# Performance work log

Measured on AMD Instinct MI355X. Metric: run time of the kernel, lower is better.

Reference implementation:

```python
import jax, jax.numpy as jnp
from jax import lax
import numpy as np

S, B, H, E, A = 1024, 32, 512, 512, 256  # seq_len, batch, hid_dim, emb_dim, att_dim


def setup_inputs() -> dict:
    key = jax.random.key(0)
    ks = jax.random.split(key, 12)
    sc = 0.02
    return {
        "outs": jax.random.normal(ks[0], (S, B, H), dtype=jnp.float32),
        "emb": jax.random.normal(ks[1], (S, B, E), dtype=jnp.float32),
        # Bahdanau scorer params: enc projection (project_enc_outs), dec projection, score vector v
        "W_enc": jax.random.normal(ks[2], (A, E), dtype=jnp.float32) * sc,
        "b_enc": jnp.zeros((A,), dtype=jnp.float32),
        "W_dec": jax.random.normal(ks[3], (A, H), dtype=jnp.float32) * sc,
        "b_dec": jnp.zeros((A,), dtype=jnp.float32),
        "v": jax.random.normal(ks[4], (A,), dtype=jnp.float32) * sc,
        # fusion linears
        "W_h2h": jax.random.normal(ks[5], (H, H), dtype=jnp.float32) * sc,
        "b_h2h": jnp.zeros((H,), dtype=jnp.float32),
        "W_e2h": jax.random.normal(ks[6], (H, E), dtype=jnp.float32) * sc,
        "b_e2h": jnp.zeros((H,), dtype=jnp.float32),
    }


def reference(outs, emb, W_enc, b_enc, W_dec, b_dec, v, W_h2h, b_h2h, W_e2h, b_e2h):
    seq = outs.shape[0]
    # project_enc_outs: (S, B, A)
    emb_att = emb @ W_enc.T + b_enc
    # per-step query index t = max(0, idx-1); context length L = max(1, t)
    idxs = jnp.arange(seq)
    t = jnp.maximum(0, idxs - 1)
    L = jnp.maximum(1, t)
    q_att = outs[t] @ W_dec.T + b_dec  # (S_q, B, A)
    # additive (Bahdanau) scores: v . tanh(q_att + emb_att); scan over queries
    # to avoid materializing the (S_q, S_k, B, A) tanh intermediate
    def step(_, qa):  # qa: (B, A)
        s = jnp.einsum("kba,a->kb", jnp.tanh(qa[None, :, :] + emb_att), v)
        return None, s
    _, scores = lax.scan(step, None, q_att)  # (S_q, S_k, B)
    # mask out keys beyond the growing context slice emb[:L]
    mask = jnp.arange(seq)[None, :] < L[:, None]  # (S_q, S_k)
    scores = jnp.where(mask[:, :, None], scores, -jnp.inf)
    weights = jax.nn.softmax(scores, axis=1)  # softmax over keys
    context = jnp.einsum("qkb,kbe->qbe", weights, emb)  # (S, B, E)
    output = outs @ W_h2h.T + b_h2h + context @ W_e2h.T + b_e2h  # (S, B, H)
    return output, weights
```

## Files before the change

### kernel.cpp

```cpp
#include <hip/hip_runtime.h>

#define Sn 1024
#define Bn 32
#define Hn 512
#define En 512
#define An 256

__global__ __launch_bounds__(256) void proj_kernel(const float* __restrict__ X,
                                                   const float* __restrict__ W,
                                                   const float* __restrict__ bias,
                                                   float* __restrict__ outp){
  __shared__ float xs[16][512];
  int tid = threadIdx.x;
  long r0 = (long)blockIdx.x * 16;
  const float4* src = (const float4*)(X + r0 * 512);
  #pragma unroll
  for (int i = 0; i < 8; i++){
    int idx = i * 256 + tid;
    float4 vv = src[idx];
    int row = idx >> 7, col = (idx & 127) * 4;
    *(float4*)&xs[row][col] = vv;
  }
  __syncthreads();
  float acc[16];
  float bz = bias[tid];
  #pragma unroll
  for (int r = 0; r < 16; r++) acc[r] = bz;
  const float4* wrow = (const float4*)(W + (long)tid * 512);
  for (int c = 0; c < 128; c += 2){
    float4 w0 = wrow[c], w1 = wrow[c + 1];
    int e0 = c * 4;
    #pragma unroll
    for (int r = 0; r < 16; r++){
      float4 x0 = *(const float4*)&xs[r][e0];
      float4 x1 = *(const float4*)&xs[r][e0 + 4];
      acc[r] += w0.x*x0.x + w0.y*x0.y + w0.z*x0.z + w0.w*x0.w
              + w1.x*x1.x + w1.y*x1.y + w1.z*x1.z + w1.w*x1.w;
    }
  }
  const float scale = 2.8853900817779268f;
  #pragma unroll
  for (int r = 0; r < 16; r++){
    long rr = r0 + r;
    int s = (int)(rr >> 5), b = (int)(rr & 31);
    outp[((long)(b * Sn + s)) * An + tid] = __builtin_amdgcn_exp2f(acc[r] * scale);
  }
}

__global__ __launch_bounds__(256) void score_kernel(const float* __restrict__ eat,
                                                    const float* __restrict__ pat,
                                                    const float* __restrict__ vptr,
                                                    float* __restrict__ wout){
  __shared__ float p[8][256];
  __shared__ float v2[256];
  __shared__ float sc[8][1024];
  int tid = threadIdx.x;
  int qt = gridDim.x - 1 - blockIdx.x;
  int b = blockIdx.y;
  #pragma unroll
  for (int q = 0; q < 8; q++){
    int qg = qt * 8 + q;
    int t = qg > 0 ? qg - 1 : 0;
    p[q][tid] = pat[((long)(b * Sn + t)) * An + tid];
  }
  float vv = vptr[tid];
  v2[tid] = 2.0f * vv;
  sc[0][tid] = vv;
  __syncthreads();
  for (int off = 128; off; off >>= 1){
    if (tid < off) sc[0][tid] += sc[0][tid + off];
    __syncthreads();
  }
  float C = sc[0][0];
  __syncthreads();
  int Lmax = qt * 8 + 6; if (Lmax < 1) Lmax = 1;
  for (int ki = 0; ki * 256 < Lmax; ki++){
    int k = ki * 256 + tid;
    if (k < Lmax){
      const float4* ep = (const float4*)(eat + ((long)(b * Sn + k)) * An);
      float acc[8] = {0,0,0,0,0,0,0,0};
      for (int c = 0; c < 32; c++){
        float4 ea = ep[2*c], eb = ep[2*c + 1];
        float e8[8] = {ea.x,ea.y,ea.z,ea.w,eb.x,eb.y,eb.z,eb.w};
        const float4* vp = (const float4*)&v2[c * 8];
        float4 va = vp[0], vb = vp[1];
        float vv8[8] = {va.x,va.y,va.z,va.w,vb.x,vb.y,vb.z,vb.w};
        #pragma unroll
        for (int q = 0; q < 8; q++){
          const float4* pp = (const float4*)&p[q][c * 8];
          float4 p0 = pp[0], p1 = pp[1];
          float pq8[8] = {p0.x,p0.y,p0.z,p0.w,p1.x,p1.y,p1.z,p1.w};
          #pragma unroll
          for (int j = 0; j < 8; j++){
            float t = __builtin_fmaf(pq8[j], e8[j], 1.0f);
            acc[q] += vv8[j] * __builtin_amdgcn_rcpf(t);
          }
        }
      }
      #pragma unroll
      for (int q = 0; q < 8; q++){
        int qg = qt * 8 + q;
        int L = qg - 1; if (L < 1) L = 1;
        sc[q][k] = (k < L) ? (C - acc[q]) : -1e30f;
      }
    }
  }
  __syncthreads();
  int g = tid >> 5, l = tid & 31;
  float m = -1e30f;
  for (int k = l; k < Lmax; k += 32) m = fmaxf(m, sc[g][k]);
  #pragma unroll
  for (int off = 16; off; off >>= 1) m = fmaxf(m, __shfl_xor(m, off, 32));
  const float LOG2E = 1.4426950408889634f;
  float ssum = 0.0f;
  for (int k = l; k < Lmax; k += 32){
    float e = __builtin_amdgcn_exp2f((sc[g][k] - m) * LOG2E);
    sc[g][k] = e; ssum += e;
  }
  #pragma unroll
  for (int off = 16; off; off >>= 1) ssum += __shfl_xor(ssum, off, 32);
  float rl = 1.0f / ssum;
  int qg = qt * 8 + g;
  for (int k = l; k < Lmax; k += 32)
    wout[((long)qg * Sn + k) * Bn + b] = sc[g][k] * rl;
}

__global__ __launch_bounds__(256) void context_kernel(const float* __restrict__ w,
                                                      const float* __restrict__ emb,
                                                      float* __restrict__ ctx){
  __shared__ float xl[8][512];
  __shared__ float wl[8][8];
  int tid = threadIdx.x;
  int qt = gridDim.x - 1 - blockIdx.x;
  int b = blockIdx.y;
  int Lmax = qt * 8 + 6; if (Lmax < 1) Lmax = 1;
  int nch = (Lmax + 7) >> 3;
  float acc[8][2];
  #pragma unroll
  for (int q = 0; q < 8; q++){ acc[q][0] = 0.f; acc[q][1] = 0.f; }
  for (int ch = 0; ch < nch; ch++){
    int k0 = ch * 8;
    __syncthreads();
    if (tid < 64){
      int q = tid >> 3, kk = tid & 7;
      wl[q][kk] = w[((long)(qt * 8 + q) * Sn + k0 + kk) * Bn + b];
    }
    #pragma unroll
    for (int i = 0; i < 4; i++){
      int idx = i * 256 + tid;
      int kr = idx >> 7, col = (idx & 127) * 4;
      const float4* src = (const float4*)(emb + ((long)((k0 + kr) * Bn + b)) * En);
      *(float4*)&xl[kr][col] = src[idx & 127];
    }
    __syncthreads();
    #pragma unroll
    for (int kk = 0; kk < 8; kk++){
      float x0 = xl[kk][tid], x1 = xl[kk][tid + 256];
      #pragma unroll
      for (int q = 0; q < 8; q++){
        float wv = wl[q][kk];
        acc[q][0] += wv * x0;
        acc[q][1] += wv * x1;
      }
    }
  }
  #pragma unroll
  for (int q = 0; q < 8; q++){
    int qg = qt * 8 + q;
    float* dst = ctx + ((long)(qg * Bn + b)) * En;
    dst[tid]       = acc[q][0];
    dst[tid + 256] = acc[q][1];
  }
}

__global__ __launch_bounds__(256) void final_kernel(const float* __restrict__ outsp,
                                                    const float* __restrict__ ctx,
                                                    const float* __restrict__ W1,
                                                    const float* __restrict__ b1,
                                                    const float* __restrict__ W2,
                                                    const float* __restrict__ b2,
                                                    float* __restrict__ outp){
  __shared__ float wl1[8][512];
  __shared__ float wl2[8][512];
  __shared__ float xl1[8][32];
  __shared__ float xl2[8][32];
  int tid = threadIdx.x;
  int rg = tid >> 6, ct = tid & 63;
  long r0 = (long)blockIdx.x * 32;

  const float4* w1a = (const float4*)(W1 + (long)tid * 512);
  const float4* w1b = (const float4*)(W1 + (long)(tid + 256) * 512);
  const float4* w2a = (const float4*)(W2 + (long)tid * 512);
  const float4* w2b = (const float4*)(W2 + (long)(tid + 256) * 512);
  int xr_ = tid & 31, xg = (tid >> 5) & 1;
  const float* xsrc = ((tid >> 6) & 1) ? ctx : outsp;
  const float* xbase = xsrc + (r0 + xr_) * 512 + xg * 4;
  float (*xl)[32] = ((tid >> 6) & 1) ? xl2 : xl1;

  float acc[8][8];
  #pragma unroll
  for (int r = 0; r < 8; r++)
    #pragma unroll
    for (int j = 0; j < 8; j++) acc[r][j] = 0.f;

  for (int c = 0; c < 64; c++){
    float4 a0 = w1a[2*c], a1 = w1a[2*c+1];
    float4 e0 = w1b[2*c], e1 = w1b[2*c+1];
    float4 f0 = w2a[2*c], f1 = w2a[2*c+1];
    float4 g0 = w2b[2*c], g1 = w2b[2*c+1];
    float4 xv;
    if (tid < 128) xv = *(const float4*)(xbase + c * 8);
    __syncthreads();
    wl1[0][tid]=a0.x; wl1[1][tid]=a0.y; wl1[2][tid]=a0.z; wl1[3][tid]=a0.w;
    wl1[4][tid]=a1.x; wl1[5][tid]=a1.y; wl1[6][tid]=a1.z; wl1[7][tid]=a1.w;
    wl1[0][tid+256]=e0.x; wl1[1][tid+256]=e0.y; wl1[2][tid+256]=e0.z; wl1[3][tid+256]=e0.w;
    wl1[4][tid+256]=e1.x; wl1[5][tid+256]=e1.y; wl1[6][tid+256]=e1.z; wl1[7][tid+256]=e1.w;
    wl2[0][tid]=f0.x; wl2[1][tid]=f0.y; wl2[2][tid]=f0.z; wl2[3][tid]=f0.w;
    wl2[4][tid]=f1.x; wl2[5][tid]=f1.y; wl2[6][tid]=f1.z; wl2[7][tid]=f1.w;
    wl2[0][tid+256]=g0.x; wl2[1][tid+256]=g0.y; wl2[2][tid+256]=g0.z; wl2[3][tid+256]=g0.w;
    wl2[4][tid+256]=g1.x; wl2[5][tid+256]=g1.y; wl2[6][tid+256]=g1.z; wl2[7][tid+256]=g1.w;
    if (tid < 128){
      xl[xg*4+0][xr_]=xv.x; xl[xg*4+1][xr_]=xv.y; xl[xg*4+2][xr_]=xv.z; xl[xg*4+3][xr_]=xv.w;
    }
    __syncthreads();
    #pragma unroll
    for (int k = 0; k < 8; k++){
      float4 xa = *(const float4*)&xl1[k][rg*8];
      float4 xb = *(const float4*)&xl1[k][rg*8+4];
      float4 ya = *(const float4*)&xl2[k][rg*8];
      float4 yb = *(const float4*)&xl2[k][rg*8+4];
      float4 wa = *(const float4*)&wl1[k][ct*4];
      float4 wb = *(const float4*)&wl1[k][256+ct*4];
      float4 va = *(const float4*)&wl2[k][ct*4];
      float4 vb = *(const float4*)&wl2[k][256+ct*4];
      float xr8[8] = {xa.x,xa.y,xa.z,xa.w,xb.x,xb.y,xb.z,xb.w};
      float yr8[8] = {ya.x,ya.y,ya.z,ya.w,yb.x,yb.y,yb.z,yb.w};
      float wc8[8] = {wa.x,wa.y,wa.z,wa.w,wb.x,wb.y,wb.z,wb.w};
      float vc8[8] = {va.x,va.y,va.z,va.w,vb.x,vb.y,vb.z,vb.w};
      #pragma unroll
      for (int r = 0; r < 8; r++)
        #pragma unroll
        for (int j = 0; j < 8; j++)
          acc[r][j] += xr8[r]*wc8[j] + yr8[r]*vc8[j];
    }
  }

  float bias[8];
  {
    float4 p0 = *(const float4*)(b1 + ct * 4);
    float4 p1 = *(const float4*)(b1 + 256 + ct * 4);
    float4 q0 = *(const float4*)(b2 + ct * 4);
    float4 q1 = *(const float4*)(b2 + 256 + ct * 4);
    bias[0]=p0.x+q0.x; bias[1]=p0.y+q0.y; bias[2]=p0.z+q0.z; bias[3]=p0.w+q0.w;
    bias[4]=p1.x+q1.x; bias[5]=p1.y+q1.y; bias[6]=p1.z+q1.z; bias[7]=p1.w+q1.w;
  }
  #pragma unroll
  for (int r = 0; r < 8; r++){
    long row = r0 + rg * 8 + r;
    float4 o0, o1;
    o0.x=acc[r][0]+bias[0]; o0.y=acc[r][1]+bias[1]; o0.z=acc[r][2]+bias[2]; o0.w=acc[r][3]+bias[3];
    o1.x=acc[r][4]+bias[4]; o1.y=acc[r][5]+bias[5]; o1.z=acc[r][6]+bias[6]; o1.w=acc[r][7]+bias[7];
    *(float4*)(outp + row * 512 + ct * 4) = o0;
    *(float4*)(outp + row * 512 + 256 + ct * 4) = o1;
  }
}

extern "C" void kernel_launch(void* const* d_in, const int* in_sizes, int n_in,
                              void* d_out, int out_size, void* d_ws, size_t ws_size,
                              hipStream_t stream) {
  const float* outs  = (const float*)d_in[0];
  const float* emb   = (const float*)d_in[1];
  const float* W_enc = (const float*)d_in[2];
  const float* b_enc = (const float*)d_in[3];
  const float* W_dec = (const float*)d_in[4];
  const float* b_dec = (const float*)d_in[5];
  const float* v     = (const float*)d_in[6];
  const float* W_h2h = (const float*)d_in[7];
  const float* b_h2h = (const float*)d_in[8];
  const float* W_e2h = (const float*)d_in[9];
  const float* b_e2h = (const float*)d_in[10];

  float* out0 = (float*)d_out;
  float* outw = out0 + (size_t)Sn * Bn * Hn;

  float* eat = out0;
  float* pat = out0 + (size_t)8388608;
  float* ctx = out0;

  hipMemsetAsync(outw, 0, (size_t)Sn * Sn * Bn * 4, stream);
  proj_kernel<<<2048, 256, 0, stream>>>(emb,  W_enc, b_enc, eat);
  proj_kernel<<<2048, 256, 0, stream>>>(outs, W_dec, b_dec, pat);
  score_kernel<<<dim3(128, 32), 256, 0, stream>>>(eat, pat, v, outw);
  context_kernel<<<dim3(128, 32), 256, 0, stream>>>(outw, emb, ctx);
  final_kernel<<<1024, 256, 0, stream>>>(outs, ctx, W_h2h, b_h2h, W_e2h, b_e2h, out0);
}
```

Before: 2.752 ms.

## Register-tile and double-buffer projection and final GEMM kernels

The projection kernel drops its row-per-thread dot product over a shared 16-row tile. It becomes a 64x256 register-tiled GEMM: 512 threads each compute an 8x4 output tile from double-buffered LDS slices of W and X, and store float4 outputs. The final fused GEMM moves to 512 threads with 64-row tiles and double-buffered LDS, so global loads for the next k-slice overlap compute on the current one. This targets the low arithmetic intensity and per-iteration sync stalls of the two linear stages, at the cost of more LDS and registers per block and fewer blocks in flight. These GEMMs are likely a small part of the total time next to the score and context kernels.

```diff
diff --git a/kernel.cpp b/kernel.cpp
--- a/kernel.cpp
+++ b/kernel.cpp
@@ -6,44 +6,85 @@
 #define En 512
 #define An 256
 
-__global__ __launch_bounds__(256) void proj_kernel(const float* __restrict__ X,
+__global__ __launch_bounds__(512) void proj_kernel(const float* __restrict__ X,
                                                    const float* __restrict__ W,
                                                    const float* __restrict__ bias,
                                                    float* __restrict__ outp){
-  __shared__ float xs[16][512];
+  __shared__ float wl[2][8][256];
+  __shared__ float xl[2][8][64];
   int tid = threadIdx.x;
-  long r0 = (long)blockIdx.x * 16;
-  const float4* src = (const float4*)(X + r0 * 512);
-  #pragma unroll
-  for (int i = 0; i < 8; i++){
-    int idx = i * 256 + tid;
-    float4 vv = src[idx];
-    int row = idx >> 7, col = (idx & 127) * 4;
-    *(float4*)&xs[row][col] = vv;
-  }
-  __syncthreads();
-  float acc[16];
-  float bz = bias[tid];
-  #pragma unroll
-  for (int r = 0; r < 16; r++) acc[r] = bz;
-  const float4* wrow = (const float4*)(W + (long)tid * 512);
-  for (int c = 0; c < 128; c += 2){
-    float4 w0 = wrow[c], w1 = wrow[c + 1];
-    int e0 = c * 4;
-    #pragma unroll
-    for (int r = 0; r < 16; r++){
-      float4 x0 = *(const float4*)&xs[r][e0];
-      float4 x1 = *(const float4*)&xs[r][e0 + 4];
-      acc[r] += w0.x*x0.x + w0.y*x0.y + w0.z*x0.z + w0.w*x0.w
-              + w1.x*x1.x + w1.y*x1.y + w1.z*x1.z + w1.w*x1.w;
-    }
-  }
+  int rg = tid >> 6;
+  int ct = tid & 63;
+  long r0 = (long)blockIdx.x * 64;
+
+  int wrow = tid >> 1, wkg = tid & 1;
+  const float* wsrc = W + (long)wrow * 512 + wkg * 4;
+  int xrow = tid >> 1, xkg = tid & 1;
+  const float* xsrc = X + (r0 + xrow) * 512 + xkg * 4;
+
+  float acc[8][4];
+  #pragma unroll
+  for (int r = 0; r < 8; r++)
+    #pragma unroll
+    for (int j = 0; j < 4; j++) acc[r][j] = 0.f;
+
+  float4 wv = *(const float4*)(wsrc);
+  float4 xv;
+  if (tid < 128) xv = *(const float4*)(xsrc);
+  wl[0][wkg*4+0][wrow]=wv.x; wl[0][wkg*4+1][wrow]=wv.y;
+  wl[0][wkg*4+2][wrow]=wv.z; wl[0][wkg*4+3][wrow]=wv.w;
+  if (tid < 128){
+    xl[0][xkg*4+0][xrow]=xv.x; xl[0][xkg*4+1][xrow]=xv.y;
+    xl[0][xkg*4+2][xrow]=xv.z; xl[0][xkg*4+3][xrow]=xv.w;
+  }
+  __syncthreads();
+
+  for (int c = 0; c < 64; c++){
+    int cb = c & 1, nb = cb ^ 1;
+    if (c < 63){
+      wv = *(const float4*)(wsrc + (c+1)*8);
+      if (tid < 128) xv = *(const float4*)(xsrc + (c+1)*8);
+    }
+    #pragma unroll
+    for (int k = 0; k < 8; k++){
+      float4 xa = *(const float4*)&xl[cb][k][rg*8];
+      float4 xb = *(const float4*)&xl[cb][k][rg*8+4];
+      float4 wc = *(const float4*)&wl[cb][k][ct*4];
+      float xr8[8] = {xa.x,xa.y,xa.z,xa.w,xb.x,xb.y,xb.z,xb.w};
+      float wc4[4] = {wc.x,wc.y,wc.z,wc.w};
+      #pragma unroll
+      for (int r = 0; r < 8; r++)
+        #pragma unroll
+        for (int j = 0; j < 4; j++)
+          acc[r][j] += xr8[r]*wc4[j];
+    }
+    if (c < 63){
+      wl[nb][wkg*4+0][wrow]=wv.x; wl[nb][wkg*4+1][wrow]=wv.y;
+      wl[nb][wkg*4+2][wrow]=wv.z; wl[nb][wkg*4+3][wrow]=wv.w;
+      if (tid < 128){
+        xl[nb][xkg*4+0][xrow]=xv.x; xl[nb][xkg*4+1][xrow]=xv.y;
+        xl[nb][xkg*4+2][xrow]=xv.z; xl[nb][xkg*4+3][xrow]=xv.w;
+      }
+    }
+    __syncthreads();
+  }
+
   const float scale = 2.8853900817779268f;
-  #pragma unroll
-  for (int r = 0; r < 16; r++){
-    long rr = r0 + r;
+  float bz[4];
+  {
+    float4 bb = *(const float4*)(bias + ct*4);
+    bz[0]=bb.x; bz[1]=bb.y; bz[2]=bb.z; bz[3]=bb.w;
+  }
+  #pragma unroll
+  for (int r = 0; r < 8; r++){
+    long rr = r0 + rg*8 + r;
     int s = (int)(rr >> 5), b = (int)(rr & 31);
-    outp[((long)(b * Sn + s)) * An + tid] = __builtin_amdgcn_exp2f(acc[r] * scale);
+    float4 o;
+    o.x = __builtin_amdgcn_exp2f((acc[r][0]+bz[0]) * scale);
+    o.y = __builtin_amdgcn_exp2f((acc[r][1]+bz[1]) * scale);
+    o.z = __builtin_amdgcn_exp2f((acc[r][2]+bz[2]) * scale);
+    o.w = __builtin_amdgcn_exp2f((acc[r][3]+bz[3]) * scale);
+    *(float4*)(outp + ((long)(b * Sn + s)) * An + ct*4) = o;
   }
 }
 
@@ -173,29 +214,28 @@
   }
 }
 
-__global__ __launch_bounds__(256) void final_kernel(const float* __restrict__ outsp,
+__global__ __launch_bounds__(512) void final_kernel(const float* __restrict__ outsp,
                                                     const float* __restrict__ ctx,
                                                     const float* __restrict__ W1,
                                                     const float* __restrict__ b1,
                                                     const float* __restrict__ W2,
                                                     const float* __restrict__ b2,
                                                     float* __restrict__ outp){
-  __shared__ float wl1[8][512];
-  __shared__ float wl2[8][512];
-  __shared__ float xl1[8][32];
-  __shared__ float xl2[8][32];
+  __shared__ float wl1[2][8][512];
+  __shared__ float wl2[2][8][512];
+  __shared__ float xl1[2][8][64];
+  __shared__ float xl2[2][8][64];
   int tid = threadIdx.x;
-  int rg = tid >> 6, ct = tid & 63;
-  long r0 = (long)blockIdx.x * 32;
-
-  const float4* w1a = (const float4*)(W1 + (long)tid * 512);
-  const float4* w1b = (const float4*)(W1 + (long)(tid + 256) * 512);
-  const float4* w2a = (const float4*)(W2 + (long)tid * 512);
-  const float4* w2b = (const float4*)(W2 + (long)(tid + 256) * 512);
-  int xr_ = tid & 31, xg = (tid >> 5) & 1;
-  const float* xsrc = ((tid >> 6) & 1) ? ctx : outsp;
-  const float* xbase = xsrc + (r0 + xr_) * 512 + xg * 4;
-  float (*xl)[32] = ((tid >> 6) & 1) ? xl2 : xl1;
+  int rg = tid >> 6;
+  int ct = tid & 63;
+  long r0 = (long)blockIdx.x * 64;
+
+  const float* wsrc1 = W1 + (long)tid * 512;
+  const float* wsrc2 = W2 + (long)tid * 512;
+  int xrow = (tid >> 1) & 63, xkg = tid & 1;
+  const float* xsrc = (tid < 128) ? (outsp + (r0 + xrow) * 512 + xkg * 4)
+                                  : (ctx   + (r0 + xrow) * 512 + xkg * 4);
+  float (*xdst)[8][64] = (tid < 128) ? xl1 : xl2;
 
   float acc[8][8];
   #pragma unroll
@@ -203,36 +243,41 @@
     #pragma unroll
     for (int j = 0; j < 8; j++) acc[r][j] = 0.f;
 
+  float4 a0 = *(const float4*)(wsrc1);
+  float4 a1 = *(const float4*)(wsrc1 + 4);
+  float4 f0 = *(const float4*)(wsrc2);
+  float4 f1 = *(const float4*)(wsrc2 + 4);
+  float4 xv;
+  if (tid < 256) xv = *(const float4*)(xsrc);
+  wl1[0][0][tid]=a0.x; wl1[0][1][tid]=a0.y; wl1[0][2][tid]=a0.z; wl1[0][3][tid]=a0.w;
+  wl1[0][4][tid]=a1.x; wl1[0][5][tid]=a1.y; wl1[0][6][tid]=a1.z; wl1[0][7][tid]=a1.w;
+  wl2[0][0][tid]=f0.x; wl2[0][1][tid]=f0.y; wl2[0][2][tid]=f0.z; wl2[0][3][tid]=f0.w;
+  wl2[0][4][tid]=f1.x; wl2[0][5][tid]=f1.y; wl2[0][6][tid]=f1.z; wl2[0][7][tid]=f1.w;
+  if (tid < 256){
+    xdst[0][xkg*4+0][xrow]=xv.x; xdst[0][xkg*4+1][xrow]=xv.y;
+    xdst[0][xkg*4+2][xrow]=xv.z; xdst[0][xkg*4+3][xrow]=xv.w;
+  }
+  __syncthreads();
+
   for (int c = 0; c < 64; c++){
-    float4 a0 = w1a[2*c], a1 = w1a[2*c+1];
-    float4 e0 = w1b[2*c], e1 = w1b[2*c+1];
-    float4 f0 = w2a[2*c], f1 = w2a[2*c+1];
-    float4 g0 = w2b[2*c], g1 = w2b[2*c+1];
-    float4 xv;
-    if (tid < 128) xv = *(const float4*)(xbase + c * 8);
-    __syncthreads();
-    wl1[0][tid]=a0.x; wl1[1][tid]=a0.y; wl1[2][tid]=a0.z; wl1[3][tid]=a0.w;
-    wl1[4][tid]=a1.x; wl1[5][tid]=a1.y; wl1[6][tid]=a1.z; wl1[7][tid]=a1.w;
-    wl1[0][tid+256]=e0.x; wl1[1][tid+256]=e0.y; wl1[2][tid+256]=e0.z; wl1[3][tid+256]=e0.w;
-    wl1[4][tid+256]=e1.x; wl1[5][tid+256]=e1.y; wl1[6][tid+256]=e1.z; wl1[7][tid+256]=e1.w;
-    wl2[0][tid]=f0.x; wl2[1][tid]=f0.y; wl2[2][tid]=f0.z; wl2[3][tid]=f0.w;
-    wl2[4][tid]=f1.x; wl2[5][tid]=f1.y; wl2[6][tid]=f1.z; wl2[7][tid]=f1.w;
-    wl2[0][tid+256]=g0.x; wl2[1][tid+256]=g0.y; wl2[2][tid+256]=g0.z; wl2[3][tid+256]=g0.w;
-    wl2[4][tid+256]=g1.x; wl2[5][tid+256]=g1.y; wl2[6][tid+256]=g1.z; wl2[7][tid+256]=g1.w;
-    if (tid < 128){
-      xl[xg*4+0][xr_]=xv.x; xl[xg*4+1][xr_]=xv.y; xl[xg*4+2][xr_]=xv.z; xl[xg*4+3][xr_]=xv.w;
-    }
-    __syncthreads();
+    int cb = c & 1, nb = cb ^ 1;
+    if (c < 63){
+      a0 = *(const float4*)(wsrc1 + (c+1)*8);
+      a1 = *(const float4*)(wsrc1 + (c+1)*8 + 4);
+      f0 = *(const float4*)(wsrc2 + (c+1)*8);
+      f1 = *(const float4*)(wsrc2 + (c+1)*8 + 4);
+      if (tid < 256) xv = *(const float4*)(xsrc + (c+1)*8);
+    }
     #pragma unroll
     for (int k = 0; k < 8; k++){
-      float4 xa = *(const float4*)&xl1[k][rg*8];
-      float4 xb = *(const float4*)&xl1[k][rg*8+4];
-      float4 ya = *(const float4*)&xl2[k][rg*8];
-      float4 yb = *(const float4*)&xl2[k][rg*8+4];
-      float4 wa = *(const float4*)&wl1[k][ct*4];
-      float4 wb = *(const float4*)&wl1[k][256+ct*4];
-      float4 va = *(const float4*)&wl2[k][ct*4];
-      float4 vb = *(const float4*)&wl2[k][256+ct*4];
+      float4 xa = *(const float4*)&xl1[cb][k][rg*8];
+      float4 xb = *(const float4*)&xl1[cb][k][rg*8+4];
+      float4 ya = *(const float4*)&xl2[cb][k][rg*8];
+      float4 yb = *(const float4*)&xl2[cb][k][rg*8+4];
+      float4 wa = *(const float4*)&wl1[cb][k][ct*4];
+      float4 wb = *(const float4*)&wl1[cb][k][256+ct*4];
+      float4 va = *(const float4*)&wl2[cb][k][ct*4];
+      float4 vb = *(const float4*)&wl2[cb][k][256+ct*4];
       float xr8[8] = {xa.x,xa.y,xa.z,xa.w,xb.x,xb.y,xb.z,xb.w};
       float yr8[8] = {ya.x,ya.y,ya.z,ya.w,yb.x,yb.y,yb.z,yb.w};
       float wc8[8] = {wa.x,wa.y,wa.z,wa.w,wb.x,wb.y,wb.z,wb.w};
@@ -243,6 +288,17 @@
         for (int j = 0; j < 8; j++)
           acc[r][j] += xr8[r]*wc8[j] + yr8[r]*vc8[j];
     }
+    if (c < 63){
+      wl1[nb][0][tid]=a0.x; wl1[nb][1][tid]=a0.y; wl1[nb][2][tid]=a0.z; wl1[nb][3][tid]=a0.w;
+      wl1[nb][4][tid]=a1.x; wl1[nb][5][tid]=a1.y; wl1[nb][6][tid]=a1.z; wl1[nb][7][tid]=a1.w;
+      wl2[nb][0][tid]=f0.x; wl2[nb][1][tid]=f0.y; wl2[nb][2][tid]=f0.z; wl2[nb][3][tid]=f0.w;
+      wl2[nb][4][tid]=f1.x; wl2[nb][5][tid]=f1.y; wl2[nb][6][tid]=f1.z; wl2[nb][7][tid]=f1.w;
+      if (tid < 256){
+        xdst[nb][xkg*4+0][xrow]=xv.x; xdst[nb][xkg*4+1][xrow]=xv.y;
+        xdst[nb][xkg*4+2][xrow]=xv.z; xdst[nb][xkg*4+3][xrow]=xv.w;
+      }
+    }
+    __syncthreads();
   }
 
   float bias[8];
@@ -288,9 +344,9 @@
   float* ctx = out0;
 
   hipMemsetAsync(outw, 0, (size_t)Sn * Sn * Bn * 4, stream);
-  proj_kernel<<<2048, 256, 0, stream>>>(emb,  W_enc, b_enc, eat);
-  proj_kernel<<<2048, 256, 0, stream>>>(outs, W_dec, b_dec, pat);
+  proj_kernel<<<512, 512, 0, stream>>>(emb,  W_enc, b_enc, eat);
+  proj_kernel<<<512, 512, 0, stream>>>(outs, W_dec, b_dec, pat);
   score_kernel<<<dim3(128, 32), 256, 0, stream>>>(eat, pat, v, outw);
   context_kernel<<<dim3(128, 32), 256, 0, stream>>>(outw, emb, ctx);
-  final_kernel<<<1024, 256, 0, stream>>>(outs, ctx, W_h2h, b_h2h, W_e2h, b_e2h, out0);
-}
+  final_kernel<<<512, 512, 0, stream>>>(outs, ctx, W_h2h, b_h2h, W_e2h, b_e2h, out0);
+}
```

After: 4.370 ms. 1.59x slower.
